# Optimization experiments

Hardware: AMD Instinct MI355X
Metric: run time of the kernel (lower is better)

## Reference

```python
import jax, jax.numpy as jnp
import numpy as np

N_QUBITS = 8
N_LAYERS = 1
DIM = 1 << N_QUBITS  # 256 statevector amplitudes; PennyLane wire 0 = most significant bit

_idx = np.arange(DIM)
_BITS = np.stack([(_idx >> (N_QUBITS - 1 - w)) & 1 for w in range(N_QUBITS)])  # (n, D)
_FLIP = np.stack([_idx ^ (1 << (N_QUBITS - 1 - w)) for w in range(N_QUBITS)])  # (n, D)

def _cnot_perm(c, t):
    return _idx ^ (((_idx >> (N_QUBITS - 1 - c)) & 1) << (N_QUBITS - 1 - t))

_CNOT_NP = [_cnot_perm(w, w + 1) for w in range(N_QUBITS - 1)] + [_cnot_perm(N_QUBITS - 1, 0)]
BITS = jnp.asarray(_BITS)
FLIP = jnp.asarray(_FLIP)
CNOTS = [jnp.asarray(p) for p in _CNOT_NP]


def _ry(t):
    c = jnp.cos(t / 2)
    s = jnp.sin(t / 2)
    return jnp.stack([jnp.stack([c, -s], -1), jnp.stack([s, c], -1)], -2).astype(jnp.complex64)


def _rx(t):
    c = jnp.cos(t / 2).astype(jnp.complex64)
    s = (-1j) * jnp.sin(t / 2).astype(jnp.complex64)
    return jnp.stack([jnp.stack([c, s], -1), jnp.stack([s, c], -1)], -2)


def _rz(t):
    tc = t.astype(jnp.complex64)
    e0 = jnp.exp(-0.5j * tc)
    e1 = jnp.exp(0.5j * tc)
    z = jnp.zeros_like(e0)
    return jnp.stack([jnp.stack([e0, z], -1), jnp.stack([z, e1], -1)], -2)


def _apply(state, U, w):
    # state: (B, 2**n) complex64; U: (2,2) shared or (B,2,2) per-sample; wire w (MSB-first)
    B = state.shape[0]
    s = state.reshape(B, 1 << w, 2, -1)
    if U.ndim == 3:
        s = jnp.einsum('bij,bajc->baic', U, s)
    else:
        s = jnp.einsum('ij,bajc->baic', U, s)
    return s.reshape(B, DIM)


def _circuit(angles, weights):
    # angles: (B, n_qubits) float32; weights: (n_layers, n_qubits, 3) float32
    B = angles.shape[0]
    state = jnp.zeros((B, DIM), jnp.complex64).at[:, 0].set(1.0)
    for w in range(N_QUBITS):
        state = _apply(state, _ry(angles[:, w]), w)  # per-sample RY encoding
    for l in range(N_LAYERS):
        for w in range(N_QUBITS):
            state = _apply(state, _rx(weights[l, w, 0]), w)
            state = _apply(state, _ry(weights[l, w, 1]), w)
            state = _apply(state, _rz(weights[l, w, 2]), w)
        for p in CNOTS:  # CNOT ring entangler as basis permutation
            state = state[:, p]
    probs = jnp.abs(state) ** 2
    outs = []
    for w in range(N_QUBITS):
        overlap = jnp.conj(state) * state[:, FLIP[w]]
        sign = (1.0 - 2.0 * BITS[w]).astype(probs.dtype)
        outs.append(jnp.sum(jnp.real(overlap), -1))       # <X_w>
        outs.append(jnp.sum(sign * jnp.imag(overlap), -1))  # <Y_w>
        outs.append(jnp.sum(sign * probs, -1))            # <Z_w>
    return jnp.stack(outs, -1)  # (B, 3*n_qubits), order X0,Y0,Z0,X1,...


def setup_inputs() -> dict:
    key = jax.random.key(0)
    k1, k2, k3 = jax.random.split(key, 3)
    B, IN_DIM = 16384, 512
    h = jax.random.normal(k1, (B, IN_DIM), jnp.float32)
    W_pre = 0.02 * jax.random.normal(k2, (N_QUBITS, IN_DIM), jnp.float32)
    b_pre = jnp.zeros((N_QUBITS,), jnp.float32)
    weights = 0.01 * jax.random.normal(k3, (N_LAYERS, N_QUBITS, 3), jnp.float32)
    return {"h": h, "W_pre": W_pre, "b_pre": b_pre, "weights": weights}


def reference(h, W_pre, b_pre, weights):
    a = h @ W_pre.T + b_pre
    a = jnp.clip(jnp.tanh(a) * (jnp.pi / 2), -jnp.pi, jnp.pi)  # _scale_to_angles
    z = _circuit(a, weights)
    norm = jnp.linalg.norm(z, axis=-1, keepdims=True)
    return z / jnp.maximum(norm, 1e-12)  # F.normalize(dim=-1)
```

## Files before the change

kernel.cpp:

```cpp
#include <hip/hip_runtime.h>


__global__ __launch_bounds__(256) void vqc_fused(
    const float* __restrict__ h,
    const float* __restrict__ Wp,
    const float* __restrict__ bp,
    const float* __restrict__ wt,
    float* __restrict__ out,
    int B)
{
    const int lane = threadIdx.x & 63;
    const int wave = (blockIdx.x * blockDim.x + threadIdx.x) >> 6;
    const int row0 = wave * 8;
    if (row0 >= B) return;

    const float4* W4 = (const float4*)Wp;
    float wf[8][8];
    #pragma unroll
    for (int q = 0; q < 8; ++q) {
        float4 v0 = W4[q * 128 + lane * 2 + 0];
        float4 v1 = W4[q * 128 + lane * 2 + 1];
        wf[q][0] = v0.x; wf[q][1] = v0.y; wf[q][2] = v0.z; wf[q][3] = v0.w;
        wf[q][4] = v1.x; wf[q][5] = v1.y; wf[q][6] = v1.z; wf[q][7] = v1.w;
    }

    const float4* H4 = (const float4*)h;
    float4 ha[8], hb[8];
    #pragma unroll
    for (int r = 0; r < 8; ++r) {
        ha[r] = H4[(row0 + r) * 128 + lane * 2 + 0];
        hb[r] = H4[(row0 + r) * 128 + lane * 2 + 1];
    }

    const int b3 = (lane >> 3) & 1, b4 = (lane >> 4) & 1, b5 = (lane >> 5) & 1;

    float v[8];
    #pragma unroll
    for (int r = 0; r < 8; ++r) {
        float hf[8] = { ha[r].x, ha[r].y, ha[r].z, ha[r].w,
                        hb[r].x, hb[r].y, hb[r].z, hb[r].w };
        float acc[8];
        #pragma unroll
        for (int q = 0; q < 8; ++q) {
            float a = 0.f;
            #pragma unroll
            for (int j = 0; j < 8; ++j) a = fmaf(wf[q][j], hf[j], a);
            acc[q] = a;
        }
        float n[4];
        #pragma unroll
        for (int j = 0; j < 4; ++j) {
            float k = b3 ? acc[1 + 2 * j] : acc[0 + 2 * j];
            float s = b3 ? acc[0 + 2 * j] : acc[1 + 2 * j];
            n[j] = k + __shfl_xor(s, 8);
        }
        float m[2];
        #pragma unroll
        for (int i = 0; i < 2; ++i) {
            float k = b4 ? n[1 + 2 * i] : n[0 + 2 * i];
            float s = b4 ? n[0 + 2 * i] : n[1 + 2 * i];
            m[i] = k + __shfl_xor(s, 16);
        }
        float k = b5 ? m[1] : m[0];
        float s = b5 ? m[0] : m[1];
        float vv = k + __shfl_xor(s, 32);
        vv += __shfl_xor(vv, 1);
        vv += __shfl_xor(vv, 2);
        vv += __shfl_xor(vv, 4);
        v[r] = vv;
    }

    float t = v[0];
    #pragma unroll
    for (int k2 = 1; k2 < 8; ++k2) t = ((lane & 7) == k2) ? v[k2] : t;

    float av[8];
    #pragma unroll
    for (int q = 0; q < 8; ++q) av[q] = __shfl(t, q * 8 + (lane & 7));

    if (lane < 8 && row0 + lane < B) {
        const int row = row0 + lane;

        float X[8], Y[8], Z[8];
        #pragma unroll
        for (int q = 0; q < 8; ++q) {
            float t0 = wt[q * 3 + 0] * 0.5f;
            float t1 = wt[q * 3 + 1] * 0.5f;
            float t2 = wt[q * 3 + 2] * 0.5f;
            float s0, c0, s1, c1, sz, cz;
            __sincosf(t0, &s0, &c0);
            __sincosf(t1, &s1, &c1);
            __sincosf(t2, &sz, &cz);
            float N00r =  c1 * c0, N00i =  s1 * s0;
            float N01r = -s1 * c0, N01i = -c1 * s0;
            float N10r =  s1 * c0, N10i = -c1 * s0;
            float N11r =  c1 * c0, N11i = -s1 * s0;
            float M00r = cz * N00r + sz * N00i, M00i = cz * N00i - sz * N00r;
            float M01r = cz * N01r + sz * N01i, M01i = cz * N01i - sz * N01r;
            float M10r = cz * N10r - sz * N10i, M10i = cz * N10i + sz * N10r;
            float M11r = cz * N11r - sz * N11i, M11i = cz * N11i + sz * N11r;

            float a = av[q] + bp[q];
            a = fminf(fmaxf(a, -15.f), 15.f);
            float e = __expf(a + a);
            float th = (e - 1.f) / (e + 1.f);
            float phi = th * 0.78539816339744831f;
            float ss, cc;
            __sincosf(phi, &ss, &cc);
            float ar = M00r * cc + M01r * ss, ai = M00i * cc + M01i * ss;
            float br = M10r * cc + M11r * ss, bi = M10i * cc + M11i * ss;
            Z[q] = (ar * ar + ai * ai) - (br * br + bi * bi);
            X[q] = 2.f * (ar * br + ai * bi);
            Y[q] = 2.f * (ar * bi - ai * br);
        }

        float P[8], T[8];
        P[0] = Z[0];
        #pragma unroll
        for (int w = 1; w < 8; ++w) P[w] = P[w - 1] * Z[w];
        T[7] = Z[7];
        #pragma unroll
        for (int w = 6; w >= 0; --w) T[w] = Z[w] * T[w + 1];
        float Z2to6 = Z[2] * Z[3] * Z[4] * Z[5] * Z[6];

        float o[24];
        #pragma unroll
        for (int w = 0; w < 7; ++w) o[3 * w] = X[w] * X[w + 1];
        o[21] = X[7] * X[0] * X[1];
        o[1] = X[0] * Y[1] * T[2];
        #pragma unroll
        for (int w = 1; w < 7; ++w) o[3 * w + 1] = Y[w] * X[w + 1] * P[w - 1];
        o[22] = -Y[7] * Y[0] * Y[1] * Z2to6;
        o[2] = T[1];
        #pragma unroll
        for (int w = 1; w < 8; ++w) o[3 * w + 2] = P[w];

        float sq = 0.f;
        #pragma unroll
        for (int j = 0; j < 24; ++j) sq = fmaf(o[j], o[j], sq);
        float inv = 1.f / fmaxf(sqrtf(sq), 1e-12f);

        float4* O4 = (float4*)(out + row * 24);
        #pragma unroll
        for (int j = 0; j < 6; ++j) {
            float4 vv = { o[4 * j] * inv, o[4 * j + 1] * inv,
                          o[4 * j + 2] * inv, o[4 * j + 3] * inv };
            O4[j] = vv;
        }
    }
}

extern "C" void kernel_launch(void* const* d_in, const int* in_sizes, int n_in,
                              void* d_out, int out_size, void* d_ws, size_t ws_size,
                              hipStream_t stream) {
    const float* h  = (const float*)d_in[0];
    const float* Wp = (const float*)d_in[1];
    const float* bp = (const float*)d_in[2];
    const float* wt = (const float*)d_in[3];
    float* out = (float*)d_out;

    const int B = in_sizes[0] / 512;
    const int waves = (B + 7) / 8;
    const int nblk = (waves + 3) / 4;
    vqc_fused<<<nblk, 256, 0, stream>>>(h, Wp, bp, wt, out, B);
}
```

Baseline: 87.38 us.

## Split fused kernel into GEMV and per-row epilogue kernels via workspace

Splits the single fused kernel into two launches: a GEMV kernel that computes the 8 projected angles per row (now 4 rows per wave instead of 8) and writes them to a workspace buffer, and an epilogue kernel with one thread per row that computes the closed-form expectation values and normalizes. The aim is to stop 56 of 64 lanes idling during the trig-heavy epilogue and to double the wave count in the bandwidth-bound GEMV. In exchange it adds a second launch and a round trip of the angle buffer through global memory.

```diff
diff --git a/kernel.cpp b/kernel.cpp
--- a/kernel.cpp
+++ b/kernel.cpp
@@ -1,17 +1,15 @@
 #include <hip/hip_runtime.h>
 
 
-__global__ __launch_bounds__(256) void vqc_fused(
+__global__ __launch_bounds__(256) void vqc_gemv(
     const float* __restrict__ h,
     const float* __restrict__ Wp,
-    const float* __restrict__ bp,
-    const float* __restrict__ wt,
-    float* __restrict__ out,
+    float* __restrict__ aw,
     int B)
 {
     const int lane = threadIdx.x & 63;
     const int wave = (blockIdx.x * blockDim.x + threadIdx.x) >> 6;
-    const int row0 = wave * 8;
+    const int row0 = wave * 4;
     if (row0 >= B) return;
 
     const float4* W4 = (const float4*)Wp;
@@ -25,18 +23,17 @@
     }
 
     const float4* H4 = (const float4*)h;
-    float4 ha[8], hb[8];
+    float4 ha[4], hb[4];
     #pragma unroll
-    for (int r = 0; r < 8; ++r) {
+    for (int r = 0; r < 4; ++r) {
         ha[r] = H4[(row0 + r) * 128 + lane * 2 + 0];
         hb[r] = H4[(row0 + r) * 128 + lane * 2 + 1];
     }
 
     const int b3 = (lane >> 3) & 1, b4 = (lane >> 4) & 1, b5 = (lane >> 5) & 1;
 
-    float v[8];
     #pragma unroll
-    for (int r = 0; r < 8; ++r) {
+    for (int r = 0; r < 4; ++r) {
         float hf[8] = { ha[r].x, ha[r].y, ha[r].z, ha[r].w,
                         hb[r].x, hb[r].y, hb[r].z, hb[r].w };
         float acc[8];
@@ -63,90 +60,95 @@
         }
         float k = b5 ? m[1] : m[0];
         float s = b5 ? m[0] : m[1];
-        float vv = k + __shfl_xor(s, 32);
-        vv += __shfl_xor(vv, 1);
-        vv += __shfl_xor(vv, 2);
-        vv += __shfl_xor(vv, 4);
-        v[r] = vv;
+        float v = k + __shfl_xor(s, 32);
+        v += __shfl_xor(v, 1);
+        v += __shfl_xor(v, 2);
+        v += __shfl_xor(v, 4);
+
+        if ((lane & 7) == 0) aw[(row0 + r) * 8 + (lane >> 3)] = v;
+    }
+}
+
+__global__ __launch_bounds__(256) void vqc_epilogue(
+    const float* __restrict__ aw,
+    const float* __restrict__ bp,
+    const float* __restrict__ wt,
+    float* __restrict__ out,
+    int B)
+{
+    const int row = blockIdx.x * blockDim.x + threadIdx.x;
+    if (row >= B) return;
+
+    const float4* A4 = (const float4*)aw;
+    float4 a0 = A4[row * 2 + 0];
+    float4 a1 = A4[row * 2 + 1];
+    float av[8] = { a0.x, a0.y, a0.z, a0.w, a1.x, a1.y, a1.z, a1.w };
+
+    float X[8], Y[8], Z[8];
+    #pragma unroll
+    for (int q = 0; q < 8; ++q) {
+        float t0 = wt[q * 3 + 0] * 0.5f;
+        float t1 = wt[q * 3 + 1] * 0.5f;
+        float t2 = wt[q * 3 + 2] * 0.5f;
+        float s0, c0, s1, c1, sz, cz;
+        __sincosf(t0, &s0, &c0);
+        __sincosf(t1, &s1, &c1);
+        __sincosf(t2, &sz, &cz);
+        float N00r =  c1 * c0, N00i =  s1 * s0;
+        float N01r = -s1 * c0, N01i = -c1 * s0;
+        float N10r =  s1 * c0, N10i = -c1 * s0;
+        float N11r =  c1 * c0, N11i = -s1 * s0;
+        float M00r = cz * N00r + sz * N00i, M00i = cz * N00i - sz * N00r;
+        float M01r = cz * N01r + sz * N01i, M01i = cz * N01i - sz * N01r;
+        float M10r = cz * N10r - sz * N10i, M10i = cz * N10i + sz * N10r;
+        float M11r = cz * N11r - sz * N11i, M11i = cz * N11i + sz * N11r;
+
+        float a = av[q] + bp[q];
+        a = fminf(fmaxf(a, -15.f), 15.f);
+        float e = __expf(a + a);
+        float th = (e - 1.f) / (e + 1.f);
+        float phi = th * 0.78539816339744831f;
+        float ss, cc;
+        __sincosf(phi, &ss, &cc);
+        float ar = M00r * cc + M01r * ss, ai = M00i * cc + M01i * ss;
+        float br = M10r * cc + M11r * ss, bi = M10i * cc + M11i * ss;
+        Z[q] = (ar * ar + ai * ai) - (br * br + bi * bi);
+        X[q] = 2.f * (ar * br + ai * bi);
+        Y[q] = 2.f * (ar * bi - ai * br);
     }
 
-    float t = v[0];
+    float P[8], T[8];
+    P[0] = Z[0];
     #pragma unroll
-    for (int k2 = 1; k2 < 8; ++k2) t = ((lane & 7) == k2) ? v[k2] : t;
+    for (int w = 1; w < 8; ++w) P[w] = P[w - 1] * Z[w];
+    T[7] = Z[7];
+    #pragma unroll
+    for (int w = 6; w >= 0; --w) T[w] = Z[w] * T[w + 1];
+    float Z2to6 = Z[2] * Z[3] * Z[4] * Z[5] * Z[6];
 
-    float av[8];
+    float o[24];
     #pragma unroll
-    for (int q = 0; q < 8; ++q) av[q] = __shfl(t, q * 8 + (lane & 7));
+    for (int w = 0; w < 7; ++w) o[3 * w] = X[w] * X[w + 1];
+    o[21] = X[7] * X[0] * X[1];
+    o[1] = X[0] * Y[1] * T[2];
+    #pragma unroll
+    for (int w = 1; w < 7; ++w) o[3 * w + 1] = Y[w] * X[w + 1] * P[w - 1];
+    o[22] = -Y[7] * Y[0] * Y[1] * Z2to6;
+    o[2] = T[1];
+    #pragma unroll
+    for (int w = 1; w < 8; ++w) o[3 * w + 2] = P[w];
 
-    if (lane < 8 && row0 + lane < B) {
-        const int row = row0 + lane;
+    float sq = 0.f;
+    #pragma unroll
+    for (int j = 0; j < 24; ++j) sq = fmaf(o[j], o[j], sq);
+    float inv = 1.f / fmaxf(sqrtf(sq), 1e-12f);
 
-        float X[8], Y[8], Z[8];
-        #pragma unroll
-        for (int q = 0; q < 8; ++q) {
-            float t0 = wt[q * 3 + 0] * 0.5f;
-            float t1 = wt[q * 3 + 1] * 0.5f;
-            float t2 = wt[q * 3 + 2] * 0.5f;
-            float s0, c0, s1, c1, sz, cz;
-            __sincosf(t0, &s0, &c0);
-            __sincosf(t1, &s1, &c1);
-            __sincosf(t2, &sz, &cz);
-            float N00r =  c1 * c0, N00i =  s1 * s0;
-            float N01r = -s1 * c0, N01i = -c1 * s0;
-            float N10r =  s1 * c0, N10i = -c1 * s0;
-            float N11r =  c1 * c0, N11i = -s1 * s0;
-            float M00r = cz * N00r + sz * N00i, M00i = cz * N00i - sz * N00r;
-            float M01r = cz * N01r + sz * N01i, M01i = cz * N01i - sz * N01r;
-            float M10r = cz * N10r - sz * N10i, M10i = cz * N10i + sz * N10r;
-            float M11r = cz * N11r - sz * N11i, M11i = cz * N11i + sz * N11r;
-
-            float a = av[q] + bp[q];
-            a = fminf(fmaxf(a, -15.f), 15.f);
-            float e = __expf(a + a);
-            float th = (e - 1.f) / (e + 1.f);
-            float phi = th * 0.78539816339744831f;
-            float ss, cc;
-            __sincosf(phi, &ss, &cc);
-            float ar = M00r * cc + M01r * ss, ai = M00i * cc + M01i * ss;
-            float br = M10r * cc + M11r * ss, bi = M10i * cc + M11i * ss;
-            Z[q] = (ar * ar + ai * ai) - (br * br + bi * bi);
-            X[q] = 2.f * (ar * br + ai * bi);
-            Y[q] = 2.f * (ar * bi - ai * br);
-        }
-
-        float P[8], T[8];
-        P[0] = Z[0];
-        #pragma unroll
-        for (int w = 1; w < 8; ++w) P[w] = P[w - 1] * Z[w];
-        T[7] = Z[7];
-        #pragma unroll
-        for (int w = 6; w >= 0; --w) T[w] = Z[w] * T[w + 1];
-        float Z2to6 = Z[2] * Z[3] * Z[4] * Z[5] * Z[6];
-
-        float o[24];
-        #pragma unroll
-        for (int w = 0; w < 7; ++w) o[3 * w] = X[w] * X[w + 1];
-        o[21] = X[7] * X[0] * X[1];
-        o[1] = X[0] * Y[1] * T[2];
-        #pragma unroll
-        for (int w = 1; w < 7; ++w) o[3 * w + 1] = Y[w] * X[w + 1] * P[w - 1];
-        o[22] = -Y[7] * Y[0] * Y[1] * Z2to6;
-        o[2] = T[1];
-        #pragma unroll
-        for (int w = 1; w < 8; ++w) o[3 * w + 2] = P[w];
-
-        float sq = 0.f;
-        #pragma unroll
-        for (int j = 0; j < 24; ++j) sq = fmaf(o[j], o[j], sq);
-        float inv = 1.f / fmaxf(sqrtf(sq), 1e-12f);
-
-        float4* O4 = (float4*)(out + row * 24);
-        #pragma unroll
-        for (int j = 0; j < 6; ++j) {
-            float4 vv = { o[4 * j] * inv, o[4 * j + 1] * inv,
-                          o[4 * j + 2] * inv, o[4 * j + 3] * inv };
-            O4[j] = vv;
-        }
+    float4* O4 = (float4*)(out + row * 24);
+    #pragma unroll
+    for (int j = 0; j < 6; ++j) {
+        float4 vv = { o[4 * j] * inv, o[4 * j + 1] * inv,
+                      o[4 * j + 2] * inv, o[4 * j + 3] * inv };
+        O4[j] = vv;
     }
 }
 
@@ -158,9 +160,11 @@
     const float* bp = (const float*)d_in[2];
     const float* wt = (const float*)d_in[3];
     float* out = (float*)d_out;
+    float* aw  = (float*)d_ws;
 
     const int B = in_sizes[0] / 512;
-    const int waves = (B + 7) / 8;
-    const int nblk = (waves + 3) / 4;
-    vqc_fused<<<nblk, 256, 0, stream>>>(h, Wp, bp, wt, out, B);
+    const int waves = (B + 3) / 4;
+    const int nblk1 = (waves + 3) / 4;
+    vqc_gemv<<<nblk1, 256, 0, stream>>>(h, Wp, aw, B);
+    vqc_epilogue<<<(B + 255) / 256, 256, 0, stream>>>(aw, bp, wt, out, B);
 }
```

Measured after the change: 83.49 us. 1.05x faster.
